# Optimization experiments

Hardware: AMD Instinct MI355X
Metric: run time of the kernel (lower is better)

The kernel has to match this reference:

```python
import jax, jax.numpy as jnp
import numpy as np

B, S, H = 2, 2048, 1024
NUM_HEAD = 16
HEAD = H // NUM_HEAD
NEG = -10000000000.0


def setup_inputs() -> dict:
    key = jax.random.key(0)
    ks = jax.random.split(key, 10)
    scale = 1.0 / np.sqrt(H)
    return {
        "query": jax.random.normal(ks[0], (B, S, H), jnp.float32),
        "key": jax.random.normal(ks[1], (B, S, H), jnp.float32),
        "value": jax.random.normal(ks[2], (B, S, H), jnp.float32),
        "mask": jax.random.randint(ks[3], (B, S), 0, 2, jnp.int32),
        "Wq": jax.random.normal(ks[4], (H, H), jnp.float32) * scale,
        "bq": jnp.zeros((H,), jnp.float32),
        "Wk": jax.random.normal(ks[5], (H, H), jnp.float32) * scale,
        "bk": jnp.zeros((H,), jnp.float32),
        "Wv": jax.random.normal(ks[6], (H, H), jnp.float32) * scale,
        "bv": jnp.zeros((H,), jnp.float32),
    }


def reference(query, key, value, mask, Wq, bq, Wk, bk, Wv, bv):
    b, s, h = query.shape
    # Linear projections (torch Linear: x @ W.T + b), split into heads -> [b, nh, s, hd]
    def proj(x, W, bias):
        y = x @ W.T + bias
        return y.reshape(b, s, NUM_HEAD, HEAD).transpose(0, 2, 1, 3)

    q = proj(query, Wq, bq)
    k = proj(key, Wk, bk)
    v = proj(value, Wv, bv)

    # NOTE: original module has NO 1/sqrt(head_dim) scaling -- faithful.
    attn_score = jnp.einsum("bhqd,bhkd->bhqk", q, k)  # [b, nh, s, s]
    # key-padding mask bias: 0 where mask==1, -1e10 where mask==0, broadcast over query dim
    bias_add = jnp.where(mask[:, None, None, :] == 0, NEG, 0.0).astype(attn_score.dtype)
    attn_score = attn_score + bias_add
    attn_ratio = jax.nn.softmax(attn_score, axis=-1)
    out = jnp.einsum("bhqk,bhkd->bhqd", attn_ratio, v)  # [b, nh, s, hd]
    out = out.transpose(0, 2, 1, 3).reshape(b, s, h)
    # Dropout is identity in eval mode; output_linear is defined but never used in forward.
    return out
```

## Files before the change

### kernel.cpp

```cpp
#include <hip/hip_runtime.h>

#define BATCH 2
#define S_LEN 2048
#define HDIM  1024
#define NHEAD 16
#define HD    64
#define NEGBIAS -1e10f
#define LOG2E 1.44269504088896f

typedef __attribute__((ext_vector_type(8))) _Float16 half8;
typedef __attribute__((ext_vector_type(4))) _Float16 half4;
typedef __attribute__((ext_vector_type(4))) float   f32x4;
typedef __attribute__((ext_vector_type(2))) __fp16 fp16x2;
typedef __attribute__((ext_vector_type(4))) __fp16 fp16x4;
typedef __attribute__((ext_vector_type(8))) __fp16 fp16x8;

__device__ __forceinline__ float max3f(float a, float b, float c) {
    return fmaxf(fmaxf(a, b), c);
}

__device__ __forceinline__ half8 pk8(float4 a, float4 b) {
    fp16x2 p0 = __builtin_amdgcn_cvt_pkrtz(a.x, a.y);
    fp16x2 p1 = __builtin_amdgcn_cvt_pkrtz(a.z, a.w);
    fp16x2 p2 = __builtin_amdgcn_cvt_pkrtz(b.x, b.y);
    fp16x2 p3 = __builtin_amdgcn_cvt_pkrtz(b.z, b.w);
    fp16x4 lo = __builtin_shufflevector(p0, p1, 0, 1, 2, 3);
    fp16x4 hi = __builtin_shufflevector(p2, p3, 0, 1, 2, 3);
    fp16x8 v8 = __builtin_shufflevector(lo, hi, 0, 1, 2, 3, 4, 5, 6, 7);
    return __builtin_bit_cast(half8, v8);
}

__device__ __forceinline__ half4 pk4(float a, float b, float c, float d) {
    fp16x2 p01 = __builtin_amdgcn_cvt_pkrtz(a, b);
    fp16x2 p23 = __builtin_amdgcn_cvt_pkrtz(c, d);
    fp16x4 v = __builtin_shufflevector(p01, p23, 0, 1, 2, 3);
    return __builtin_bit_cast(half4, v);
}

__global__ __launch_bounds__(256) void proj_gemm_f16(
    const float* __restrict__ Xq, const float* __restrict__ Wq, const float* __restrict__ bq,
    const float* __restrict__ Xk, const float* __restrict__ Wk, const float* __restrict__ bk,
    const float* __restrict__ Xv, const float* __restrict__ Wv, const float* __restrict__ bv,
    _Float16* __restrict__ Qb, _Float16* __restrict__ Kb, _Float16* __restrict__ Vtb)
{
    const int z = blockIdx.z;
    const float* X    = (z == 0) ? Xq : (z == 1) ? Xk : Xv;
    const float* W    = (z == 0) ? Wq : (z == 1) ? Wk : Wv;
    const float* bias = (z == 0) ? bq : (z == 1) ? bk : bv;
    _Float16* Y       = (z == 0) ? Qb : (z == 1) ? Kb : Vtb;

    const int n0 = blockIdx.x * 128;
    const int m0 = blockIdx.y * 128;

    __shared__ __align__(16) _Float16 As[128][40];
    __shared__ __align__(16) _Float16 Bs[128][40];

    const int t    = threadIdx.x;
    const int w    = t >> 6;
    const int lane = t & 63;
    const int quad = lane >> 4;
    const int lc   = lane & 15;
    const int wm   = (w >> 1) * 64;
    const int wn   = (w & 1) * 64;

    const f32x4 fzero = {0.f, 0.f, 0.f, 0.f};
    f32x4 acc[4][4];
#pragma unroll
    for (int i = 0; i < 4; i++)
#pragma unroll
        for (int j2 = 0; j2 < 4; j2++) acc[i][j2] = fzero;

    const int srow = t >> 2;
    const int sc   = t & 3;

    float4 xa[2][2], wa[2][2];
#define PROJ_ISSUE(K0)                                                        \
    {                                                                         \
        _Pragma("unroll")                                                     \
        for (int hf = 0; hf < 2; hf++) {                                      \
            const float* gx = X + (size_t)(m0 + srow + hf * 64) * HDIM + (K0) + sc * 8; \
            xa[hf][0] = *(const float4*)gx;                                   \
            xa[hf][1] = *(const float4*)(gx + 4);                             \
            const float* gw = W + (size_t)(n0 + srow + hf * 64) * HDIM + (K0) + sc * 8; \
            wa[hf][0] = *(const float4*)gw;                                   \
            wa[hf][1] = *(const float4*)(gw + 4);                             \
        }                                                                     \
    }

    PROJ_ISSUE(0)

    for (int k0 = 0; k0 < HDIM; k0 += 32) {
        if (k0) __syncthreads();
#pragma unroll
        for (int hf = 0; hf < 2; hf++) {
            int row = srow + hf * 64;
            *(half8*)&As[row][sc * 8] = pk8(xa[hf][0], xa[hf][1]);
            *(half8*)&Bs[row][sc * 8] = pk8(wa[hf][0], wa[hf][1]);
        }
        __syncthreads();

        if (k0 + 32 < HDIM) PROJ_ISSUE(k0 + 32)

        half8 af[4], bf[4];
#pragma unroll
        for (int mt = 0; mt < 4; mt++)
            af[mt] = *(const half8*)&As[wm + mt * 16 + lc][quad * 8];
#pragma unroll
        for (int nt = 0; nt < 4; nt++)
            bf[nt] = *(const half8*)&Bs[wn + nt * 16 + lc][quad * 8];
#pragma unroll
        for (int mt = 0; mt < 4; mt++)
#pragma unroll
            for (int nt = 0; nt < 4; nt++)
                acc[mt][nt] = __builtin_amdgcn_mfma_f32_16x16x32_f16(
                    af[mt], bf[nt], acc[mt][nt], 0, 0, 0);
    }

#pragma unroll
    for (int nt = 0; nt < 4; nt++) {
        const int n = n0 + wn + nt * 16 + lc;
        const float bv_ = bias[n];
        const int h = n >> 6, d = n & 63;
#pragma unroll
        for (int mt = 0; mt < 4; mt++) {
            if (z == 2) {
                const int m = m0 + wm + mt * 16 + quad * 4;
                const int b = m >> 11, s = m & (S_LEN - 1);
                const int bh = b * NHEAD + h;
                half4 v = pk4(acc[mt][nt][0] + bv_, acc[mt][nt][1] + bv_,
                              acc[mt][nt][2] + bv_, acc[mt][nt][3] + bv_);
                *(half4*)&Vtb[((size_t)bh * HD + d) * S_LEN + s] = v;
            } else {
#pragma unroll
                for (int r = 0; r < 4; r++) {
                    const int m = m0 + wm + mt * 16 + quad * 4 + r;
                    const int b = m >> 11, s = m & (S_LEN - 1);
                    const int bh = b * NHEAD + h;
                    float y = acc[mt][nt][r] + bv_;
                    if (z == 0) y *= LOG2E;
                    Y[((size_t)bh * S_LEN + s) * HD + d] = (_Float16)y;
                }
            }
        }
    }
}

__global__ __launch_bounds__(256) void flash_attn_mfma(
    const _Float16* __restrict__ Qb, const _Float16* __restrict__ Kb,
    const _Float16* __restrict__ Vtb, const int* __restrict__ mask,
    float* __restrict__ out)
{
    const int bid = blockIdx.x;
    const int swz = (bid & 7) * 64 + (bid >> 3);
    const int qt = swz & 15;
    const int bh = swz >> 4;
    const int b  = bh >> 4;
    const int h  = bh & (NHEAD - 1);

    __shared__ __align__(16) _Float16 Ks [64][72];
    __shared__ __align__(16) _Float16 Vts[64][72];
    __shared__ __align__(16) _Float16 Ps [4][32][72];

    const int t    = threadIdx.x;
    const int w    = t >> 6;
    const int lane = t & 63;
    const int quad = lane >> 4;
    const int lc   = lane & 15;

    const _Float16* Kbase = Kb  + (size_t)bh * S_LEN * HD;
    const _Float16* Vbase = Vtb + (size_t)bh * HD * S_LEN;
    const int*      ml    = mask + b * S_LEN + quad * 4;

    half8 qf[2][2];
#pragma unroll
    for (int qg = 0; qg < 2; qg++) {
        const int qrow = qt * 128 + w * 32 + qg * 16 + lc;
#pragma unroll
        for (int s = 0; s < 2; s++)
            qf[qg][s] = *(const half8*)(Qb + ((size_t)bh * S_LEN + qrow) * HD
                                        + s * 32 + quad * 8);
    }

    f32x4 o[2][4];
    const f32x4 fzero = {0.f, 0.f, 0.f, 0.f};
#pragma unroll
    for (int qg = 0; qg < 2; qg++)
#pragma unroll
        for (int nt = 0; nt < 4; nt++) o[qg][nt] = fzero;
    float mrun[2] = {-3.0e38f, -3.0e38f};
    float lrun[2] = {0.f, 0.f};

    const int rr0 = t >> 3,          cc0 = (t & 7) * 8;
    const int rr1 = (t + 256) >> 3;

    half8 kpre[2], vpre[2];
#define ATTN_ISSUE(KT)                                                        \
    {                                                                         \
        kpre[0] = *(const half8*)(Kbase + (size_t)((KT) + rr0) * HD + cc0);   \
        kpre[1] = *(const half8*)(Kbase + (size_t)((KT) + rr1) * HD + cc0);   \
        vpre[0] = *(const half8*)(Vbase + (size_t)rr0 * S_LEN + (KT) + cc0);  \
        vpre[1] = *(const half8*)(Vbase + (size_t)rr1 * S_LEN + (KT) + cc0);  \
    }

    ATTN_ISSUE(0)

    for (int kt = 0; kt < S_LEN; kt += 64) {
        if (kt) __syncthreads();
        *(half8*)&Ks [rr0][cc0] = kpre[0];
        *(half8*)&Ks [rr1][cc0] = kpre[1];
        *(half8*)&Vts[rr0][cc0] = vpre[0];
        *(half8*)&Vts[rr1][cc0] = vpre[1];
        __syncthreads();

        if (kt + 64 < S_LEN) ATTN_ISSUE(kt + 64)

        int4 mm[4];
#pragma unroll
        for (int tt = 0; tt < 4; tt++)
            mm[tt] = *(const int4*)(ml + kt + tt * 16);

        f32x4 scf[2][4];
#pragma unroll
        for (int tt = 0; tt < 4; tt++) {
            f32x4 cini;
            cini[0] = mm[tt].x ? 0.f : NEGBIAS;
            cini[1] = mm[tt].y ? 0.f : NEGBIAS;
            cini[2] = mm[tt].z ? 0.f : NEGBIAS;
            cini[3] = mm[tt].w ? 0.f : NEGBIAS;
            scf[0][tt] = cini;
            scf[1][tt] = cini;
        }
#pragma unroll
        for (int s = 0; s < 2; s++) {
#pragma unroll
            for (int tt = 0; tt < 4; tt++) {
                half8 kf = *(const half8*)&Ks[tt * 16 + lc][s * 32 + quad * 8];
                scf[0][tt] = __builtin_amdgcn_mfma_f32_16x16x32_f16(kf, qf[0][s], scf[0][tt], 0, 0, 0);
                scf[1][tt] = __builtin_amdgcn_mfma_f32_16x16x32_f16(kf, qf[1][s], scf[1][tt], 0, 0, 0);
            }
        }

#pragma unroll
        for (int qg = 0; qg < 2; qg++) {
            const f32x4 a0 = scf[qg][0], a1 = scf[qg][1],
                        a2 = scf[qg][2], a3 = scf[qg][3];
            float m0 = max3f(a0[0], a0[1], a0[2]);
            float m1 = max3f(a0[3], a1[0], a1[1]);
            float m2 = max3f(a1[2], a1[3], a2[0]);
            float m3 = max3f(a2[1], a2[2], a2[3]);
            float m4 = max3f(a3[0], a3[1], a3[2]);
            float mx = fmaxf(max3f(m0, m1, m2), max3f(m3, m4, a3[3]));
            mx = fmaxf(mx, __shfl_xor(mx, 16));
            mx = fmaxf(mx, __shfl_xor(mx, 32));

            if (!__all(mx <= mrun[qg] + 8.f)) {
                float mn = fmaxf(mrun[qg], mx);
                float al = __builtin_amdgcn_exp2f(mrun[qg] - mn);
                lrun[qg] *= al;
#pragma unroll
                for (int nt = 0; nt < 4; nt++) {
                    o[qg][nt][0] *= al; o[qg][nt][1] *= al;
                    o[qg][nt][2] *= al; o[qg][nt][3] *= al;
                }
                mrun[qg] = mn;
            }

            const float mr = mrun[qg];
            float ps[4][4];
#pragma unroll
            for (int tt = 0; tt < 4; tt++)
#pragma unroll
                for (int r = 0; r < 4; r++) {
                    float p = __builtin_amdgcn_exp2f(scf[qg][tt][r] - mr);
                    ps[tt][r] = p;
                }
            float s0 = (ps[0][0] + ps[0][1]) + (ps[0][2] + ps[0][3]);
            float s1 = (ps[1][0] + ps[1][1]) + (ps[1][2] + ps[1][3]);
            float s2 = (ps[2][0] + ps[2][1]) + (ps[2][2] + ps[2][3]);
            float s3 = (ps[3][0] + ps[3][1]) + (ps[3][2] + ps[3][3]);
            float ls = (s0 + s1) + (s2 + s3);
            ls += __shfl_xor(ls, 16);
            ls += __shfl_xor(ls, 32);
            lrun[qg] += ls;

#pragma unroll
            for (int tt = 0; tt < 4; tt++) {
                *(half4*)&Ps[w][qg * 16 + lc][tt * 16 + quad * 4] =
                    pk4(ps[tt][0], ps[tt][1], ps[tt][2], ps[tt][3]);
            }
        }

#pragma unroll
        for (int s = 0; s < 2; s++) {
            half8 pf0 = *(const half8*)&Ps[w][lc]     [s * 32 + quad * 8];
            half8 pf1 = *(const half8*)&Ps[w][16 + lc][s * 32 + quad * 8];
#pragma unroll
            for (int nt = 0; nt < 4; nt++) {
                half8 vf = *(const half8*)&Vts[nt * 16 + lc][s * 32 + quad * 8];
                o[0][nt] = __builtin_amdgcn_mfma_f32_16x16x32_f16(vf, pf0, o[0][nt], 0, 0, 0);
                o[1][nt] = __builtin_amdgcn_mfma_f32_16x16x32_f16(vf, pf1, o[1][nt], 0, 0, 0);
            }
        }
    }

#pragma unroll
    for (int qg = 0; qg < 2; qg++) {
        const int qrow = qt * 128 + w * 32 + qg * 16 + lc;
        const float inv = 1.f / lrun[qg];
        const size_t rowb = ((size_t)b * S_LEN + qrow) * HDIM + h * HD;
#pragma unroll
        for (int nt = 0; nt < 4; nt++) {
            float4 v;
            v.x = o[qg][nt][0] * inv; v.y = o[qg][nt][1] * inv;
            v.z = o[qg][nt][2] * inv; v.w = o[qg][nt][3] * inv;
            *(float4*)&out[rowb + nt * 16 + quad * 4] = v;
        }
    }
}

extern "C" void kernel_launch(void* const* d_in, const int* in_sizes, int n_in,
                              void* d_out, int out_size, void* d_ws, size_t ws_size,
                              hipStream_t stream) {
    const float* query = (const float*)d_in[0];
    const float* key   = (const float*)d_in[1];
    const float* value = (const float*)d_in[2];
    const int*   mask  = (const int*)  d_in[3];
    const float* Wq    = (const float*)d_in[4];
    const float* bq    = (const float*)d_in[5];
    const float* Wk    = (const float*)d_in[6];
    const float* bk    = (const float*)d_in[7];
    const float* Wv    = (const float*)d_in[8];
    const float* bv    = (const float*)d_in[9];
    float* out = (float*)d_out;

    const size_t nElem = (size_t)BATCH * S_LEN * HDIM;
    if (ws_size < 3 * nElem * sizeof(_Float16)) return;
    _Float16* Qb  = (_Float16*)d_ws;
    _Float16* Kb  = Qb + nElem;
    _Float16* Vtb = Kb + nElem;

    dim3 gproj(HDIM / 128, (BATCH * S_LEN) / 128, 3);
    proj_gemm_f16<<<gproj, 256, 0, stream>>>(query, Wq, bq, key, Wk, bk,
                                             value, Wv, bv, Qb, Kb, Vtb);

    flash_attn_mfma<<<BATCH * NHEAD * (S_LEN / 128), 256, 0, stream>>>(
        Qb, Kb, Vtb, mask, out);
}
```

Baseline: 235.8 us.

## Double K-step depth in projection GEMM and attention tiles, stage mask bias in LDS

The projection GEMM now stages 64-wide K slices per iteration instead of 32 and runs two MFMA sub-steps per sync. The attention kernel loads 128 keys per iteration into larger LDS tiles and processes them in two 64-key halves. It also precomputes the mask bias once per tile into shared memory instead of each thread reading the mask from global memory. This halves the number of barriers and global load rounds, but raises register pressure from the larger prefetch buffers and increases LDS use, which may lower occupancy.

```diff
diff --git a/kernel.cpp b/kernel.cpp
--- a/kernel.cpp
+++ b/kernel.cpp
@@ -52,8 +52,8 @@
     const int n0 = blockIdx.x * 128;
     const int m0 = blockIdx.y * 128;
 
-    __shared__ __align__(16) _Float16 As[128][40];
-    __shared__ __align__(16) _Float16 Bs[128][40];
+    __shared__ __align__(16) _Float16 As[128][72];
+    __shared__ __align__(16) _Float16 Bs[128][72];
 
     const int t    = threadIdx.x;
     const int w    = t >> 6;
@@ -70,50 +70,55 @@
 #pragma unroll
         for (int j2 = 0; j2 < 4; j2++) acc[i][j2] = fzero;
 
-    const int srow = t >> 2;
-    const int sc   = t & 3;
-
-    float4 xa[2][2], wa[2][2];
+    const int sr = t >> 3;
+    const int sk = (t & 7) * 8;
+
+    float4 xa[4][2], wa[4][2];
 #define PROJ_ISSUE(K0)                                                        \
     {                                                                         \
         _Pragma("unroll")                                                     \
-        for (int hf = 0; hf < 2; hf++) {                                      \
-            const float* gx = X + (size_t)(m0 + srow + hf * 64) * HDIM + (K0) + sc * 8; \
-            xa[hf][0] = *(const float4*)gx;                                   \
-            xa[hf][1] = *(const float4*)(gx + 4);                             \
-            const float* gw = W + (size_t)(n0 + srow + hf * 64) * HDIM + (K0) + sc * 8; \
-            wa[hf][0] = *(const float4*)gw;                                   \
-            wa[hf][1] = *(const float4*)(gw + 4);                             \
+        for (int i = 0; i < 4; i++) {                                         \
+            const float* gx = X + (size_t)(m0 + sr + 32 * i) * HDIM + (K0) + sk; \
+            xa[i][0] = *(const float4*)gx;                                    \
+            xa[i][1] = *(const float4*)(gx + 4);                              \
+            const float* gw = W + (size_t)(n0 + sr + 32 * i) * HDIM + (K0) + sk; \
+            wa[i][0] = *(const float4*)gw;                                    \
+            wa[i][1] = *(const float4*)(gw + 4);                              \
         }                                                                     \
     }
 
+#define PROJ_COMP(HF)                                                         \
+    {                                                                         \
+        half8 af[4], bf[4];                                                   \
+        _Pragma("unroll")                                                     \
+        for (int mt = 0; mt < 4; mt++)                                        \
+            af[mt] = *(const half8*)&As[wm + mt * 16 + lc][(HF) * 32 + quad * 8]; \
+        _Pragma("unroll")                                                     \
+        for (int nt = 0; nt < 4; nt++)                                        \
+            bf[nt] = *(const half8*)&Bs[wn + nt * 16 + lc][(HF) * 32 + quad * 8]; \
+        _Pragma("unroll")                                                     \
+        for (int mt = 0; mt < 4; mt++)                                        \
+            _Pragma("unroll")                                                 \
+            for (int nt = 0; nt < 4; nt++)                                    \
+                acc[mt][nt] = __builtin_amdgcn_mfma_f32_16x16x32_f16(         \
+                    af[mt], bf[nt], acc[mt][nt], 0, 0, 0);                    \
+    }
+
     PROJ_ISSUE(0)
 
-    for (int k0 = 0; k0 < HDIM; k0 += 32) {
+    for (int k0 = 0; k0 < HDIM; k0 += 64) {
         if (k0) __syncthreads();
 #pragma unroll
-        for (int hf = 0; hf < 2; hf++) {
-            int row = srow + hf * 64;
-            *(half8*)&As[row][sc * 8] = pk8(xa[hf][0], xa[hf][1]);
-            *(half8*)&Bs[row][sc * 8] = pk8(wa[hf][0], wa[hf][1]);
+        for (int i = 0; i < 4; i++) {
+            *(half8*)&As[sr + 32 * i][sk] = pk8(xa[i][0], xa[i][1]);
+            *(half8*)&Bs[sr + 32 * i][sk] = pk8(wa[i][0], wa[i][1]);
         }
         __syncthreads();
 
-        if (k0 + 32 < HDIM) PROJ_ISSUE(k0 + 32)
-
-        half8 af[4], bf[4];
-#pragma unroll
-        for (int mt = 0; mt < 4; mt++)
-            af[mt] = *(const half8*)&As[wm + mt * 16 + lc][quad * 8];
-#pragma unroll
-        for (int nt = 0; nt < 4; nt++)
-            bf[nt] = *(const half8*)&Bs[wn + nt * 16 + lc][quad * 8];
-#pragma unroll
-        for (int mt = 0; mt < 4; mt++)
-#pragma unroll
-            for (int nt = 0; nt < 4; nt++)
-                acc[mt][nt] = __builtin_amdgcn_mfma_f32_16x16x32_f16(
-                    af[mt], bf[nt], acc[mt][nt], 0, 0, 0);
+        if (k0 + 64 < HDIM) PROJ_ISSUE(k0 + 64)
+
+        PROJ_COMP(0)
+        PROJ_COMP(1)
     }
 
 #pragma unroll
@@ -157,9 +162,10 @@
     const int b  = bh >> 4;
     const int h  = bh & (NHEAD - 1);
 
-    __shared__ __align__(16) _Float16 Ks [64][72];
-    __shared__ __align__(16) _Float16 Vts[64][72];
+    __shared__ __align__(16) _Float16 Ks [128][72];
+    __shared__ __align__(16) _Float16 Vts[64][136];
     __shared__ __align__(16) _Float16 Ps [4][32][72];
+    __shared__ float biasS[128];
 
     const int t    = threadIdx.x;
     const int w    = t >> 6;
@@ -169,7 +175,7 @@
 
     const _Float16* Kbase = Kb  + (size_t)bh * S_LEN * HD;
     const _Float16* Vbase = Vtb + (size_t)bh * HD * S_LEN;
-    const int*      ml    = mask + b * S_LEN + quad * 4;
+    const int* mbase = mask + b * S_LEN;
 
     half8 qf[2][2];
 #pragma unroll
@@ -190,115 +196,115 @@
     float mrun[2] = {-3.0e38f, -3.0e38f};
     float lrun[2] = {0.f, 0.f};
 
-    const int rr0 = t >> 3,          cc0 = (t & 7) * 8;
-    const int rr1 = (t + 256) >> 3;
-
-    half8 kpre[2], vpre[2];
+    const int kr = t >> 3,  kc = (t & 7) * 8;
+    const int vr = t >> 4,  vc = (t & 15) * 8;
+
+    half8 kpre[4], vpre[4];
+    int   mpre;
 #define ATTN_ISSUE(KT)                                                        \
     {                                                                         \
-        kpre[0] = *(const half8*)(Kbase + (size_t)((KT) + rr0) * HD + cc0);   \
-        kpre[1] = *(const half8*)(Kbase + (size_t)((KT) + rr1) * HD + cc0);   \
-        vpre[0] = *(const half8*)(Vbase + (size_t)rr0 * S_LEN + (KT) + cc0);  \
-        vpre[1] = *(const half8*)(Vbase + (size_t)rr1 * S_LEN + (KT) + cc0);  \
+        _Pragma("unroll")                                                     \
+        for (int i = 0; i < 4; i++) {                                         \
+            kpre[i] = *(const half8*)(Kbase + (size_t)((KT) + kr + 32 * i) * HD + kc); \
+            vpre[i] = *(const half8*)(Vbase + (size_t)(vr + 16 * i) * S_LEN + (KT) + vc); \
+        }                                                                     \
+        mpre = mbase[(KT) + (t & 127)];                                       \
     }
 
     ATTN_ISSUE(0)
 
-    for (int kt = 0; kt < S_LEN; kt += 64) {
+    for (int kt = 0; kt < S_LEN; kt += 128) {
         if (kt) __syncthreads();
-        *(half8*)&Ks [rr0][cc0] = kpre[0];
-        *(half8*)&Ks [rr1][cc0] = kpre[1];
-        *(half8*)&Vts[rr0][cc0] = vpre[0];
-        *(half8*)&Vts[rr1][cc0] = vpre[1];
+#pragma unroll
+        for (int i = 0; i < 4; i++) {
+            *(half8*)&Ks [kr + 32 * i][kc] = kpre[i];
+            *(half8*)&Vts[vr + 16 * i][vc] = vpre[i];
+        }
+        if (t < 128) biasS[t] = mpre ? 0.f : NEGBIAS;
         __syncthreads();
 
-        if (kt + 64 < S_LEN) ATTN_ISSUE(kt + 64)
-
-        int4 mm[4];
-#pragma unroll
-        for (int tt = 0; tt < 4; tt++)
-            mm[tt] = *(const int4*)(ml + kt + tt * 16);
-
-        f32x4 scf[2][4];
-#pragma unroll
-        for (int tt = 0; tt < 4; tt++) {
-            f32x4 cini;
-            cini[0] = mm[tt].x ? 0.f : NEGBIAS;
-            cini[1] = mm[tt].y ? 0.f : NEGBIAS;
-            cini[2] = mm[tt].z ? 0.f : NEGBIAS;
-            cini[3] = mm[tt].w ? 0.f : NEGBIAS;
-            scf[0][tt] = cini;
-            scf[1][tt] = cini;
-        }
-#pragma unroll
-        for (int s = 0; s < 2; s++) {
+        if (kt + 128 < S_LEN) ATTN_ISSUE(kt + 128)
+
+#pragma unroll
+        for (int hf = 0; hf < 2; hf++) {
+            f32x4 scf[2][4];
 #pragma unroll
             for (int tt = 0; tt < 4; tt++) {
-                half8 kf = *(const half8*)&Ks[tt * 16 + lc][s * 32 + quad * 8];
-                scf[0][tt] = __builtin_amdgcn_mfma_f32_16x16x32_f16(kf, qf[0][s], scf[0][tt], 0, 0, 0);
-                scf[1][tt] = __builtin_amdgcn_mfma_f32_16x16x32_f16(kf, qf[1][s], scf[1][tt], 0, 0, 0);
-            }
-        }
-
-#pragma unroll
-        for (int qg = 0; qg < 2; qg++) {
-            const f32x4 a0 = scf[qg][0], a1 = scf[qg][1],
-                        a2 = scf[qg][2], a3 = scf[qg][3];
-            float m0 = max3f(a0[0], a0[1], a0[2]);
-            float m1 = max3f(a0[3], a1[0], a1[1]);
-            float m2 = max3f(a1[2], a1[3], a2[0]);
-            float m3 = max3f(a2[1], a2[2], a2[3]);
-            float m4 = max3f(a3[0], a3[1], a3[2]);
-            float mx = fmaxf(max3f(m0, m1, m2), max3f(m3, m4, a3[3]));
-            mx = fmaxf(mx, __shfl_xor(mx, 16));
-            mx = fmaxf(mx, __shfl_xor(mx, 32));
-
-            if (!__all(mx <= mrun[qg] + 8.f)) {
-                float mn = fmaxf(mrun[qg], mx);
-                float al = __builtin_amdgcn_exp2f(mrun[qg] - mn);
-                lrun[qg] *= al;
+                float4 b4 = *(const float4*)&biasS[hf * 64 + tt * 16 + quad * 4];
+                f32x4 cini = {b4.x, b4.y, b4.z, b4.w};
+                scf[0][tt] = cini;
+                scf[1][tt] = cini;
+            }
+#pragma unroll
+            for (int s = 0; s < 2; s++) {
+#pragma unroll
+                for (int tt = 0; tt < 4; tt++) {
+                    half8 kf = *(const half8*)&Ks[hf * 64 + tt * 16 + lc][s * 32 + quad * 8];
+                    scf[0][tt] = __builtin_amdgcn_mfma_f32_16x16x32_f16(kf, qf[0][s], scf[0][tt], 0, 0, 0);
+                    scf[1][tt] = __builtin_amdgcn_mfma_f32_16x16x32_f16(kf, qf[1][s], scf[1][tt], 0, 0, 0);
+                }
+            }
+
+#pragma unroll
+            for (int qg = 0; qg < 2; qg++) {
+                const f32x4 a0 = scf[qg][0], a1 = scf[qg][1],
+                            a2 = scf[qg][2], a3 = scf[qg][3];
+                float m0 = max3f(a0[0], a0[1], a0[2]);
+                float m1 = max3f(a0[3], a1[0], a1[1]);
+                float m2 = max3f(a1[2], a1[3], a2[0]);
+                float m3 = max3f(a2[1], a2[2], a2[3]);
+                float m4 = max3f(a3[0], a3[1], a3[2]);
+                float mx = fmaxf(max3f(m0, m1, m2), max3f(m3, m4, a3[3]));
+                mx = fmaxf(mx, __shfl_xor(mx, 16));
+                mx = fmaxf(mx, __shfl_xor(mx, 32));
+
+                if (!__all(mx <= mrun[qg] + 8.f)) {
+                    float mn = fmaxf(mrun[qg], mx);
+                    float al = __builtin_amdgcn_exp2f(mrun[qg] - mn);
+                    lrun[qg] *= al;
+#pragma unroll
+                    for (int nt = 0; nt < 4; nt++) {
+                        o[qg][nt][0] *= al; o[qg][nt][1] *= al;
+                        o[qg][nt][2] *= al; o[qg][nt][3] *= al;
+                    }
+                    mrun[qg] = mn;
+                }
+
+                const float mr = mrun[qg];
+                float ps[4][4];
+#pragma unroll
+                for (int tt = 0; tt < 4; tt++)
+#pragma unroll
+                    for (int r = 0; r < 4; r++) {
+                        float p = __builtin_amdgcn_exp2f(scf[qg][tt][r] - mr);
+                        ps[tt][r] = p;
+                    }
+                float s0 = (ps[0][0] + ps[0][1]) + (ps[0][2] + ps[0][3]);
+                float s1 = (ps[1][0] + ps[1][1]) + (ps[1][2] + ps[1][3]);
+                float s2 = (ps[2][0] + ps[2][1]) + (ps[2][2] + ps[2][3]);
+                float s3 = (ps[3][0] + ps[3][1]) + (ps[3][2] + ps[3][3]);
+                float ls = (s0 + s1) + (s2 + s3);
+                ls += __shfl_xor(ls, 16);
+                ls += __shfl_xor(ls, 32);
+                lrun[qg] += ls;
+
+#pragma unroll
+                for (int tt = 0; tt < 4; tt++) {
+                    *(half4*)&Ps[w][qg * 16 + lc][tt * 16 + quad * 4] =
+                        pk4(ps[tt][0], ps[tt][1], ps[tt][2], ps[tt][3]);
+                }
+            }
+
+#pragma unroll
+            for (int s = 0; s < 2; s++) {
+                half8 pf0 = *(const half8*)&Ps[w][lc]     [s * 32 + quad * 8];
+                half8 pf1 = *(const half8*)&Ps[w][16 + lc][s * 32 + quad * 8];
 #pragma unroll
                 for (int nt = 0; nt < 4; nt++) {
-                    o[qg][nt][0] *= al; o[qg][nt][1] *= al;
-                    o[qg][nt][2] *= al; o[qg][nt][3] *= al;
-                }
-                mrun[qg] = mn;
-            }
-
-            const float mr = mrun[qg];
-            float ps[4][4];
-#pragma unroll
-            for (int tt = 0; tt < 4; tt++)
-#pragma unroll
-                for (int r = 0; r < 4; r++) {
-                    float p = __builtin_amdgcn_exp2f(scf[qg][tt][r] - mr);
-                    ps[tt][r] = p;
-                }
-            float s0 = (ps[0][0] + ps[0][1]) + (ps[0][2] + ps[0][3]);
-            float s1 = (ps[1][0] + ps[1][1]) + (ps[1][2] + ps[1][3]);
-            float s2 = (ps[2][0] + ps[2][1]) + (ps[2][2] + ps[2][3]);
-            float s3 = (ps[3][0] + ps[3][1]) + (ps[3][2] + ps[3][3]);
-            float ls = (s0 + s1) + (s2 + s3);
-            ls += __shfl_xor(ls, 16);
-            ls += __shfl_xor(ls, 32);
-            lrun[qg] += ls;
-
-#pragma unroll
-            for (int tt = 0; tt < 4; tt++) {
-                *(half4*)&Ps[w][qg * 16 + lc][tt * 16 + quad * 4] =
-                    pk4(ps[tt][0], ps[tt][1], ps[tt][2], ps[tt][3]);
-            }
-        }
-
-#pragma unroll
-        for (int s = 0; s < 2; s++) {
-            half8 pf0 = *(const half8*)&Ps[w][lc]     [s * 32 + quad * 8];
-            half8 pf1 = *(const half8*)&Ps[w][16 + lc][s * 32 + quad * 8];
-#pragma unroll
-            for (int nt = 0; nt < 4; nt++) {
-                half8 vf = *(const half8*)&Vts[nt * 16 + lc][s * 32 + quad * 8];
-                o[0][nt] = __builtin_amdgcn_mfma_f32_16x16x32_f16(vf, pf0, o[0][nt], 0, 0, 0);
-                o[1][nt] = __builtin_amdgcn_mfma_f32_16x16x32_f16(vf, pf1, o[1][nt], 0, 0, 0);
+                    half8 vf = *(const half8*)&Vts[nt * 16 + lc][hf * 64 + s * 32 + quad * 8];
+                    o[0][nt] = __builtin_amdgcn_mfma_f32_16x16x32_f16(vf, pf0, o[0][nt], 0, 0, 0);
+                    o[1][nt] = __builtin_amdgcn_mfma_f32_16x16x32_f16(vf, pf1, o[1][nt], 0, 0, 0);
+                }
             }
         }
     }
```

Result: no change. 237.2 us (+0.6%).
